# Performance work log

Hardware: AMD Instinct MI355X
Metric: run time of the kernel (lower is better)

The kernel has to match this reference:

```python
import jax, jax.numpy as jnp
import numpy as np

NUM_SPLITS = 2  # attn_splits


def _split_c_last(x, ns):
    # split_feature(channel_last=True): [b,h,w,c] -> [b*ns*ns, h/ns, w/ns, c]
    b, h, w, c = x.shape
    x = x.reshape(b, ns, h // ns, ns, w // ns, c)
    x = jnp.transpose(x, (0, 1, 3, 2, 4, 5))
    return x.reshape(b * ns * ns, h // ns, w // ns, c)


def _merge_c_last(x, ns):
    # merge_splits(channel_last=True): [b*ns*ns, hh, ww, c] -> [b, ns*hh, ns*ww, c]
    bn, hh, ww, c = x.shape
    b = bn // (ns * ns)
    x = x.reshape(b, ns, ns, hh, ww, c)
    x = jnp.transpose(x, (0, 1, 3, 2, 4, 5))
    return x.reshape(b, ns * hh, ns * ww, c)


def _make_shift_window_mask(h, w, ns):
    # exact port of generate_shift_window_attn_mask (numpy, setup-time only)
    wh, ww = h // ns, w // ns
    sh, sw = wh // 2, ww // 2
    img = np.zeros((h, w))
    cnt = 0
    for hs in (slice(0, -wh), slice(-wh, -sh), slice(-sh, None)):
        for ws in (slice(0, -ww), slice(-ww, -sw), slice(-sw, None)):
            img[hs, ws] = cnt
            cnt += 1
    mw = img.reshape(ns, wh, ns, ww).transpose(0, 2, 1, 3).reshape(ns * ns, wh * ww)
    am = mw[:, None, :] - mw[:, :, None]  # [n, i, j] = mw[n, j] - mw[n, i]
    am = np.where(am != 0, -100.0, 0.0).astype(np.float32)
    return jnp.asarray(am)


def _window_attention(q, k, v, attn_mask, h, w, ns):
    # single_head_split_window_attention with with_shift=True
    b, hw, c = q.shape
    sh, sw = (h // ns) // 2, (w // ns) // 2

    def prep(x):
        x = x.reshape(b, h, w, c)
        x = jnp.roll(x, shift=(-sh, -sw), axis=(1, 2))
        return _split_c_last(x, ns).reshape(b * ns * ns, -1, c)

    qs, ks, vs = prep(q), prep(k), prep(v)
    scale = jnp.asarray(c, q.dtype) ** 0.5
    scores = jnp.einsum('bqc,bkc->bqk', qs, ks) / scale
    scores = scores + jnp.tile(attn_mask, (b, 1, 1))
    attn = jax.nn.softmax(scores, axis=-1)
    out = jnp.einsum('bqk,bkc->bqc', attn, vs)
    out = _merge_c_last(out.reshape(b * ns * ns, h // ns, w // ns, c), ns)
    out = jnp.roll(out, shift=(sh, sw), axis=(1, 2))
    return out.reshape(b, hw, c)


def _global_correlation_softmax(feature0, feature1):
    b, c, h, w = feature0.shape
    hw = h * w
    f0 = feature0.reshape(b, c, hw).transpose(0, 2, 1)  # [b, hw, c]
    f1 = feature1.reshape(b, c, hw)                     # [b, c, hw]
    scale = jnp.asarray(c, feature0.dtype) ** 0.5
    corr = jnp.matmul(f0, f1) / scale                   # [b, hw, hw]

    yy, xx = jnp.meshgrid(jnp.arange(h), jnp.arange(w), indexing='ij')
    init_grid = jnp.stack([xx, yy], axis=0).astype(feature0.dtype)  # [2,h,w]
    init_grid = jnp.broadcast_to(init_grid[None], (b, 2, h, w))
    grid = init_grid.reshape(b, 2, hw).transpose(0, 2, 1)            # [b, hw, 2]

    corr2 = jnp.concatenate([corr, jnp.transpose(corr, (0, 2, 1))], axis=0)  # [2b,hw,hw]
    grid2 = jnp.tile(grid, (2, 1, 1))
    init2 = jnp.tile(init_grid, (2, 1, 1, 1))

    prob = jax.nn.softmax(corr2, axis=-1)
    corresp = jnp.matmul(prob, grid2).reshape(2 * b, h, w, 2)
    corresp = jnp.transpose(corresp, (0, 3, 1, 2))
    flow = corresp - init2
    f01, f10 = flow[:b], flow[b:]
    dual_prob = prob[:b] * jnp.transpose(prob[b:], (0, 2, 1))
    return f01, f10, dual_prob


def setup_inputs() -> dict:
    key = jax.random.key(0)
    b, c, h, w = 2, 128, 48, 96
    ks = jax.random.split(key, 5)
    q = jax.random.normal(ks[0], (b, h * w, c), dtype=jnp.float32)
    k = jax.random.normal(ks[1], (b, h * w, c), dtype=jnp.float32)
    v = jax.random.normal(ks[2], (b, h * w, c), dtype=jnp.float32)
    feature0 = jax.random.normal(ks[3], (b, c, h, w), dtype=jnp.float32)
    feature1 = jax.random.normal(ks[4], (b, c, h, w), dtype=jnp.float32)
    attn_mask = _make_shift_window_mask(h, w, NUM_SPLITS)
    return {"q": q, "k": k, "v": v, "feature0": feature0, "feature1": feature1,
            "attn_mask": attn_mask, "h": h, "w": w}


def reference(q, k, v, feature0, feature1, attn_mask, h, w):
    attn_out = _window_attention(q, k, v, attn_mask, h, w, NUM_SPLITS)
    f01, f10, dual_prob = _global_correlation_softmax(feature0, feature1)
    return (attn_out, f01, f10, dual_prob)
```

## Files before the change

kernel.cpp:

```cpp
#include <hip/hip_runtime.h>

#define HW 4608
#define CC 128
#define H 48
#define W 96
#define S_WIN 1152
#define SCALE 0.08838834764831845f

typedef __attribute__((ext_vector_type(8))) short bf16x8;
typedef __attribute__((ext_vector_type(4))) float f32x4;

static __device__ inline short f2bf(float f) {
    unsigned u = __builtin_bit_cast(unsigned, f);
    unsigned r = (u + 0x7fff + ((u >> 16) & 1)) >> 16;
    return (short)r;
}

__global__ __launch_bounds__(256)
void prep_all(const float* __restrict__ Q, const float* __restrict__ K, const float* __restrict__ V,
              const float* __restrict__ f0, const float* __restrict__ f1,
              bf16x8* __restrict__ cfragA, bf16x8* __restrict__ cfragB,
              bf16x8* __restrict__ qfrag, bf16x8* __restrict__ kfrag, bf16x8* __restrict__ vfrag,
              float* __restrict__ wsf)
{
    __shared__ float vt[32][132];
    const int bx = blockIdx.x;
    const int t = threadIdx.x;

    if (bx < 1152) {
        int zi = bx * 256 + t;
        if (zi < 12 * HW) wsf[zi] = 0.f;
        const int pt = bx % 72;
        const int z  = bx / 72;
        const int tensor = z >> 3, b = (z >> 2) & 1, kc = z & 3;
        const float* src = (tensor ? f1 : f0) + (size_t)b * CC * HW + (size_t)kc * 32 * HW + pt * 64;
        {
            int ch = t >> 4;
            int c4 = (t & 15) * 4;
            *(float4*)&vt[ch][c4]      = *(const float4*)&src[(size_t)ch * HW + c4];
            *(float4*)&vt[ch + 16][c4] = *(const float4*)&src[(size_t)(ch + 16) * HW + c4];
        }
        __syncthreads();
        int Rloc = t >> 6, lane = t & 63;
        int R = pt * 4 + Rloc;
        bf16x8 v;
        #pragma unroll
        for (int j = 0; j < 8; ++j) v[j] = f2bf(vt[(lane >> 4) * 8 + j][Rloc * 16 + (lane & 15)]);
        (tensor ? cfragB : cfragA)[((size_t)(b * 288 + R) * 4 + kc) * 64 + lane] = v;
    } else {
        const int bx2 = bx - 1152;
        const int R2 = bx2 % 36;
        const int z  = bx2 / 36;
        const int tensor = z >> 3, wb = z & 7;
        const int bb = wb >> 2, wi = wb & 3, si = wi >> 1, sj = wi & 1;
        const float* src = (tensor == 0 ? Q : (tensor == 1 ? K : V)) + (size_t)bb * HW * CC;
        {
            int row = t >> 3;
            int c16 = (t & 7) * 16;
            int qw = R2 * 32 + row;
            int rr = qw / 48, cc = qw - rr * 48;
            int y = (si * 24 + rr + 12) % 48;
            int x = (sj * 48 + cc + 24) % 96;
            const float* rp = src + ((size_t)y * 96 + x) * CC + c16;
            #pragma unroll
            for (int u = 0; u < 4; ++u)
                *(float4*)&vt[row][c16 + u * 4] = *(const float4*)&rp[u * 4];
        }
        __syncthreads();
        if (tensor < 2) {
            bf16x8* frag = tensor == 0 ? qfrag : kfrag;
            #pragma unroll
            for (int e2 = 0; e2 < 2; ++e2) {
                int e = t + e2 * 256;
                int Rloc = e >> 8, kc = (e >> 6) & 3, lane = e & 63;
                int R = R2 * 2 + Rloc;
                bf16x8 v;
                #pragma unroll
                for (int j = 0; j < 8; ++j)
                    v[j] = f2bf(vt[Rloc * 16 + (lane & 15)][kc * 32 + (lane >> 4) * 8 + j]);
                frag[((size_t)(wb * 72 + R) * 4 + kc) * 64 + lane] = v;
            }
        } else {
            #pragma unroll
            for (int e2 = 0; e2 < 2; ++e2) {
                int e = t + e2 * 256;
                int dB = e >> 6, lane = e & 63;
                bf16x8 v;
                #pragma unroll
                for (int j = 0; j < 8; ++j)
                    v[j] = f2bf(vt[(lane >> 4) * 8 + j][dB * 16 + (lane & 15)]);
                vfrag[((size_t)(wb * 8 + dB) * 36 + R2) * 64 + lane] = v;
            }
        }
    }
}

__global__ __launch_bounds__(512)
void win_attn(const bf16x8* __restrict__ qfrag, const bf16x8* __restrict__ kfrag,
              const bf16x8* __restrict__ vfrag, float* __restrict__ out)
{
    __shared__ __align__(16) short Psh[16 * 1152];
    __shared__ unsigned char codes[S_WIN];
    __shared__ float rsum_sh[16];

    const int t = threadIdx.x, lane = t & 63, w = t >> 6;
    const int qt = blockIdx.x;
    const int wb = blockIdx.y;
    const int bb = wb >> 2, wi = wb & 3, si = wi >> 1, sj = wi & 1;

    if (t < 16) rsum_sh[t] = 0.f;
    for (int i = t; i < S_WIN; i += 512) {
        int r = i / 48, c = i - r * 48;
        codes[i] = (unsigned char)((si ? (r >= 12) : 0) | ((sj ? (c >= 24) : 0) << 1));
    }
    __syncthreads();

    bf16x8 qf[4];
    {
        const bf16x8* qb = qfrag + ((size_t)(wb * 72 + qt) * 4) * 64 + lane;
        #pragma unroll
        for (int kc = 0; kc < 4; ++kc) qf[kc] = qb[kc * 64];
    }
    const int qcode = codes[qt * 16 + (lane & 15)];
    char* Pb = (char*)Psh;
    float rsum = 0.f;

    for (int kt = 0; kt < 9; ++kt) {
        int Rk = w * 9 + kt;
        const bf16x8* kb = kfrag + ((size_t)(wb * 72 + Rk) * 4) * 64 + lane;
        bf16x8 kf[4];
        #pragma unroll
        for (int kc = 0; kc < 4; ++kc) kf[kc] = kb[kc * 64];
        int k0 = Rk * 16 + (lane >> 4) * 4;
        f32x4 acc = {0.f, 0.f, 0.f, 0.f};
        #pragma unroll
        for (int kc = 0; kc < 4; ++kc)
            acc = __builtin_amdgcn_mfma_f32_16x16x32_bf16(kf[kc], qf[kc], acc, 0, 0, 0);
        float ev[4];
        #pragma unroll
        for (int r = 0; r < 4; ++r) {
            ev[r] = (codes[k0 + r] == qcode) ? __expf(acc[r] * SCALE) : 0.f;
            rsum += ev[r];
        }
        unsigned lo = (unsigned)(unsigned short)f2bf(ev[0]) | ((unsigned)(unsigned short)f2bf(ev[1]) << 16);
        unsigned hi = (unsigned)(unsigned short)f2bf(ev[2]) | ((unsigned)(unsigned short)f2bf(ev[3]) << 16);
        int qloc = lane & 15;
        int off = (qloc * 2304 + k0 * 2) ^ ((qloc & 7) << 4);
        *(uint2*)(Pb + off) = make_uint2(lo, hi);
    }
    rsum += __shfl_xor(rsum, 16); rsum += __shfl_xor(rsum, 32);
    if (lane < 16) atomicAdd(&rsum_sh[lane], rsum);
    __syncthreads();

    f32x4 pv = {0.f, 0.f, 0.f, 0.f};
    const bf16x8* vb = vfrag + ((size_t)(wb * 8 + w) * 36) * 64 + lane;
    for (int kc = 0; kc < 36; ++kc) {
        int qloc = lane & 15;
        int off = (qloc * 2304 + kc * 64 + (lane >> 4) * 16) ^ ((qloc & 7) << 4);
        bf16x8 pf = *(const bf16x8*)(Pb + off);
        pv = __builtin_amdgcn_mfma_f32_16x16x32_bf16(pf, vb[kc * 64], pv, 0, 0, 0);
    }
    #pragma unroll
    for (int r = 0; r < 4; ++r) {
        int qloc = (lane >> 4) * 4 + r;
        float val = pv[r] / rsum_sh[qloc];
        int qw = qt * 16 + qloc;
        int rr = qw / 48, cc2 = qw - rr * 48;
        int y = (si * 24 + rr + 12) % 48;
        int x = (sj * 48 + cc2 + 24) % 96;
        out[((size_t)bb * HW + y * 96 + x) * CC + w * 16 + (lane & 15)] = val;
    }
}

__global__ __launch_bounds__(256)
void corr_stats(const bf16x8* __restrict__ fragA, const bf16x8* __restrict__ fragB,
                float* __restrict__ rowsum, float* __restrict__ colsum)
{
    __shared__ float rs[128], cs[128];
    const int t = threadIdx.x, lane = t & 63, wave = t >> 6;
    const int wm = wave >> 1, wn = wave & 1;
    const int kt = blockIdx.x, qt = blockIdx.y, b = blockIdx.z;

    const bf16x8* Ab = fragA + (size_t)(b * 288 + qt * 8 + wm * 4) * 256 + lane;
    const bf16x8* Bb = fragB + (size_t)(b * 288 + kt * 8 + wn * 4) * 256 + lane;

    f32x4 acc[4][4] = {};
    #pragma unroll
    for (int kc = 0; kc < 4; ++kc) {
        bf16x8 a[4], bf[4];
        #pragma unroll
        for (int m = 0; m < 4; ++m) a[m]  = Ab[(m * 4 + kc) * 64];
        #pragma unroll
        for (int n = 0; n < 4; ++n) bf[n] = Bb[(n * 4 + kc) * 64];
        #pragma unroll
        for (int m = 0; m < 4; ++m)
            #pragma unroll
            for (int n = 0; n < 4; ++n)
                acc[m][n] = __builtin_amdgcn_mfma_f32_16x16x32_bf16(a[m], bf[n], acc[m][n], 0, 0, 0);
    }

    if (t < 128) { rs[t] = 0.f; cs[t] = 0.f; }
    __syncthreads();

    float cv[4] = {};
    #pragma unroll
    for (int m = 0; m < 4; ++m) {
        float rv[4] = {};
        #pragma unroll
        for (int n = 0; n < 4; ++n)
            #pragma unroll
            for (int r = 0; r < 4; ++r) {
                float ev = __expf(acc[m][n][r] * SCALE);
                rv[r] += ev; cv[n] += ev;
            }
        #pragma unroll
        for (int r = 0; r < 4; ++r) {
            float s = rv[r];
            s += __shfl_xor(s, 1); s += __shfl_xor(s, 2);
            s += __shfl_xor(s, 4); s += __shfl_xor(s, 8);
            if ((lane & 15) == 0)
                atomicAdd(&rs[wm * 64 + m * 16 + (lane >> 4) * 4 + r], s);
        }
    }
    #pragma unroll
    for (int n = 0; n < 4; ++n) {
        float s = cv[n];
        s += __shfl_xor(s, 16); s += __shfl_xor(s, 32);
        if (lane < 16) atomicAdd(&cs[wn * 64 + n * 16 + lane], s);
    }
    __syncthreads();
    if (t < 128)      atomicAdd(&rowsum[(size_t)b * HW + qt * 128 + t], rs[t]);
    else              atomicAdd(&colsum[(size_t)b * HW + kt * 128 + (t - 128)], cs[t - 128]);
}

__global__ __launch_bounds__(256)
void corr_final(const bf16x8* __restrict__ fragA, const bf16x8* __restrict__ fragB,
                const float* __restrict__ rowsum, const float* __restrict__ colsum,
                float* __restrict__ rowflow, float* __restrict__ colflow,
                float* __restrict__ dual)
{
    __shared__ float sfx[128], sfy[128], scx[128], scy[128];
    __shared__ float stg[4][16][68];
    const int t = threadIdx.x, lane = t & 63, wave = t >> 6;
    const int wm = wave >> 1, wn = wave & 1;
    const int kt = blockIdx.x, qt = blockIdx.y, b = blockIdx.z;

    const bf16x8* Ab = fragA + (size_t)(b * 288 + qt * 8 + wm * 4) * 256 + lane;
    const bf16x8* Bb = fragB + (size_t)(b * 288 + kt * 8 + wn * 4) * 256 + lane;

    f32x4 acc[4][4] = {};
    #pragma unroll
    for (int kc = 0; kc < 4; ++kc) {
        bf16x8 a[4], bf[4];
        #pragma unroll
        for (int m = 0; m < 4; ++m) a[m]  = Ab[(m * 4 + kc) * 64];
        #pragma unroll
        for (int n = 0; n < 4; ++n) bf[n] = Bb[(n * 4 + kc) * 64];
        #pragma unroll
        for (int m = 0; m < 4; ++m)
            #pragma unroll
            for (int n = 0; n < 4; ++n)
                acc[m][n] = __builtin_amdgcn_mfma_f32_16x16x32_bf16(a[m], bf[n], acc[m][n], 0, 0, 0);
    }

    if (t < 128) { sfx[t] = 0.f; sfy[t] = 0.f; scx[t] = 0.f; scy[t] = 0.f; }
    __syncthreads();

    const int qbase = qt * 128 + wm * 64;
    const int kbase = kt * 128 + wn * 64;

    float cinv[4], gkx[4], gky[4];
    #pragma unroll
    for (int n = 0; n < 4; ++n) {
        int k = kbase + n * 16 + (lane & 15);
        cinv[n] = 1.f / colsum[(size_t)b * HW + k];
        int kyi = k / W;
        gkx[n] = (float)(k - kyi * W); gky[n] = (float)kyi;
    }

    float cfx[4] = {}, cfy[4] = {};
    #pragma unroll
    for (int m = 0; m < 4; ++m) {
        float rinv[4], gqx[4], gqy[4];
        int q0 = qbase + m * 16 + (lane >> 4) * 4;
        #pragma unroll
        for (int r = 0; r < 4; ++r) {
            rinv[r] = 1.f / rowsum[(size_t)b * HW + q0 + r];
            int qyi = (q0 + r) / W;
            gqx[r] = (float)(q0 + r - qyi * W); gqy[r] = (float)qyi;
        }
        float rfx[4] = {}, rfy[4] = {};
        #pragma unroll
        for (int n = 0; n < 4; ++n) {
            #pragma unroll
            for (int r = 0; r < 4; ++r) {
                float ev = __expf(acc[m][n][r] * SCALE);
                float rp = ev * rinv[r];
                float ce = ev * cinv[n];
                stg[wave][(lane >> 4) * 4 + r][n * 16 + (lane & 15)] = rp * ce;
                rfx[r] += rp * gkx[n]; rfy[r] += rp * gky[n];
                cfx[n] += ce * gqx[r]; cfy[n] += ce * gqy[r];
            }
        }
        #pragma unroll
        for (int pass = 0; pass < 4; ++pass) {
            int row = pass * 4 + (lane >> 4);
            float4 vv = *(const float4*)&stg[wave][row][(lane & 15) * 4];
            *(float4*)&dual[((size_t)b * HW + qbase + m * 16 + row) * HW + kbase + (lane & 15) * 4] = vv;
        }
        #pragma unroll
        for (int r = 0; r < 4; ++r) {
            float sx = rfx[r], sy = rfy[r];
            sx += __shfl_xor(sx, 1); sx += __shfl_xor(sx, 2);
            sx += __shfl_xor(sx, 4); sx += __shfl_xor(sx, 8);
            sy += __shfl_xor(sy, 1); sy += __shfl_xor(sy, 2);
            sy += __shfl_xor(sy, 4); sy += __shfl_xor(sy, 8);
            if ((lane & 15) == 0) {
                int row = wm * 64 + m * 16 + (lane >> 4) * 4 + r;
                atomicAdd(&sfx[row], sx); atomicAdd(&sfy[row], sy);
            }
        }
    }
    #pragma unroll
    for (int n = 0; n < 4; ++n) {
        float sx = cfx[n], sy = cfy[n];
        sx += __shfl_xor(sx, 16); sx += __shfl_xor(sx, 32);
        sy += __shfl_xor(sy, 16); sy += __shfl_xor(sy, 32);
        if (lane < 16) {
            int col = wn * 64 + n * 16 + lane;
            atomicAdd(&scx[col], sx); atomicAdd(&scy[col], sy);
        }
    }
    __syncthreads();
    if (t < 128) {
        atomicAdd(&rowflow[((size_t)b * HW + qt * 128 + t) * 2 + 0], sfx[t]);
        atomicAdd(&rowflow[((size_t)b * HW + qt * 128 + t) * 2 + 1], sfy[t]);
    } else {
        int j = t - 128;
        atomicAdd(&colflow[((size_t)b * HW + kt * 128 + j) * 2 + 0], scx[j]);
        atomicAdd(&colflow[((size_t)b * HW + kt * 128 + j) * 2 + 1], scy[j]);
    }
}

__global__ void flow_finalize(const float* __restrict__ rowflow, const float* __restrict__ colflow,
                              float* __restrict__ out)
{
    int i = blockIdx.x * 256 + threadIdx.x;
    if (i >= 2 * 2 * HW) return;
    int bb   = i / (2 * HW);
    int rem  = i % (2 * HW);
    int chan = rem / HW;
    int q    = rem % HW;
    float g = (chan == 0) ? (float)(q % W) : (float)(q / W);
    out[i]              = rowflow[((size_t)bb * HW + q) * 2 + chan] - g;
    out[2 * 2 * HW + i] = colflow[((size_t)bb * HW + q) * 2 + chan] - g;
}

extern "C" void kernel_launch(void* const* d_in, const int* in_sizes, int n_in,
                              void* d_out, int out_size, void* d_ws, size_t ws_size,
                              hipStream_t stream)
{
    (void)in_sizes; (void)n_in; (void)out_size; (void)ws_size;
    const float* q  = (const float*)d_in[0];
    const float* k  = (const float*)d_in[1];
    const float* v  = (const float*)d_in[2];
    const float* f0 = (const float*)d_in[3];
    const float* f1 = (const float*)d_in[4];

    float* out = (float*)d_out;
    const size_t ATTN_SZ = (size_t)2 * HW * CC;
    const size_t FLOW_SZ = (size_t)2 * 2 * HW;
    float* f01  = out + ATTN_SZ;
    float* dual = out + ATTN_SZ + 2 * FLOW_SZ;

    const size_t FR = 2359296;
    char* wsb = (char*)d_ws;
    bf16x8* cfragA = (bf16x8*)(wsb);
    bf16x8* cfragB = (bf16x8*)(wsb + FR);
    bf16x8* qfrag  = (bf16x8*)(wsb + 2 * FR);
    bf16x8* kfrag  = (bf16x8*)(wsb + 3 * FR);
    bf16x8* vfrag  = (bf16x8*)(wsb + 4 * FR);
    float* wsf     = (float*)(wsb + 5 * FR);
    float* rowsum  = wsf;
    float* colsum  = wsf + 2 * HW;
    float* rowflow = wsf + 4 * HW;
    float* colflow = wsf + 8 * HW;

    prep_all<<<dim3(2016), 256, 0, stream>>>(q, k, v, f0, f1, cfragA, cfragB,
                                             qfrag, kfrag, vfrag, wsf);
    win_attn<<<dim3(72, 8), 512, 0, stream>>>(qfrag, kfrag, vfrag, out);
    corr_stats<<<dim3(36, 36, 2), 256, 0, stream>>>(cfragA, cfragB, rowsum, colsum);
    corr_final<<<dim3(36, 36, 2), 256, 0, stream>>>(cfragA, cfragB, rowsum, colsum,
                                                    rowflow, colflow, dual);
    flow_finalize<<<dim3(72), 256, 0, stream>>>(rowflow, colflow, f01);
}
```

Baseline: 133.8 us.

## Merge window attention and correlation stats into one launch; nontemporal dual stores

Combines the window-attention kernel and the correlation row/column-sum kernel into a single launch by splitting the block index range. The attention part now runs 256 threads per block, with each wave doing twice the key tiles and two output column tiles. This removes one launch and lets the two independent workloads fill the GPU together. Separately, the large dual-probability output is written with nontemporal stores to reduce cache pollution. The fused kernel's register pressure and shared-memory footprint apply to both halves, which may change occupancy.

```diff
diff --git a/kernel.cpp b/kernel.cpp
--- a/kernel.cpp
+++ b/kernel.cpp
@@ -95,142 +95,147 @@
     }
 }
 
-__global__ __launch_bounds__(512)
-void win_attn(const bf16x8* __restrict__ qfrag, const bf16x8* __restrict__ kfrag,
-              const bf16x8* __restrict__ vfrag, float* __restrict__ out)
+__global__ __launch_bounds__(256)
+void fused_ws(const bf16x8* __restrict__ qfrag, const bf16x8* __restrict__ kfrag,
+              const bf16x8* __restrict__ vfrag, float* __restrict__ out,
+              const bf16x8* __restrict__ cfragA, const bf16x8* __restrict__ cfragB,
+              float* __restrict__ rowsum, float* __restrict__ colsum)
 {
-    __shared__ __align__(16) short Psh[16 * 1152];
-    __shared__ unsigned char codes[S_WIN];
-    __shared__ float rsum_sh[16];
-
+    __shared__ __align__(16) char smem[38144];
+    const int bx = blockIdx.x;
     const int t = threadIdx.x, lane = t & 63, w = t >> 6;
-    const int qt = blockIdx.x;
-    const int wb = blockIdx.y;
-    const int bb = wb >> 2, wi = wb & 3, si = wi >> 1, sj = wi & 1;
-
-    if (t < 16) rsum_sh[t] = 0.f;
-    for (int i = t; i < S_WIN; i += 512) {
-        int r = i / 48, c = i - r * 48;
-        codes[i] = (unsigned char)((si ? (r >= 12) : 0) | ((sj ? (c >= 24) : 0) << 1));
-    }
-    __syncthreads();
-
-    bf16x8 qf[4];
-    {
-        const bf16x8* qb = qfrag + ((size_t)(wb * 72 + qt) * 4) * 64 + lane;
-        #pragma unroll
-        for (int kc = 0; kc < 4; ++kc) qf[kc] = qb[kc * 64];
-    }
-    const int qcode = codes[qt * 16 + (lane & 15)];
-    char* Pb = (char*)Psh;
-    float rsum = 0.f;
-
-    for (int kt = 0; kt < 9; ++kt) {
-        int Rk = w * 9 + kt;
-        const bf16x8* kb = kfrag + ((size_t)(wb * 72 + Rk) * 4) * 64 + lane;
-        bf16x8 kf[4];
-        #pragma unroll
-        for (int kc = 0; kc < 4; ++kc) kf[kc] = kb[kc * 64];
-        int k0 = Rk * 16 + (lane >> 4) * 4;
-        f32x4 acc = {0.f, 0.f, 0.f, 0.f};
-        #pragma unroll
-        for (int kc = 0; kc < 4; ++kc)
-            acc = __builtin_amdgcn_mfma_f32_16x16x32_bf16(kf[kc], qf[kc], acc, 0, 0, 0);
-        float ev[4];
+
+    if (bx < 576) {
+        short* Psh = (short*)smem;
+        unsigned char* codes = (unsigned char*)(smem + 36864);
+        float* rsum_sh = (float*)(smem + 38016);
+        const int qt = bx % 72, wb = bx / 72;
+        const int bb = wb >> 2, wi = wb & 3, si = wi >> 1, sj = wi & 1;
+
+        if (t < 16) rsum_sh[t] = 0.f;
+        for (int i = t; i < S_WIN; i += 256) {
+            int r = i / 48, c = i - r * 48;
+            codes[i] = (unsigned char)((si ? (r >= 12) : 0) | ((sj ? (c >= 24) : 0) << 1));
+        }
+        __syncthreads();
+
+        bf16x8 qf[4];
+        {
+            const bf16x8* qb = qfrag + ((size_t)(wb * 72 + qt) * 4) * 64 + lane;
+            #pragma unroll
+            for (int kc = 0; kc < 4; ++kc) qf[kc] = qb[kc * 64];
+        }
+        const int qcode = codes[qt * 16 + (lane & 15)];
+        char* Pb = (char*)Psh;
+        float rsum = 0.f;
+
+        for (int kt = 0; kt < 18; ++kt) {
+            int Rk = w * 18 + kt;
+            const bf16x8* kb = kfrag + ((size_t)(wb * 72 + Rk) * 4) * 64 + lane;
+            bf16x8 kf[4];
+            #pragma unroll
+            for (int kc = 0; kc < 4; ++kc) kf[kc] = kb[kc * 64];
+            int k0 = Rk * 16 + (lane >> 4) * 4;
+            f32x4 acc = {0.f, 0.f, 0.f, 0.f};
+            #pragma unroll
+            for (int kc = 0; kc < 4; ++kc)
+                acc = __builtin_amdgcn_mfma_f32_16x16x32_bf16(kf[kc], qf[kc], acc, 0, 0, 0);
+            float ev[4];
+            #pragma unroll
+            for (int r = 0; r < 4; ++r) {
+                ev[r] = (codes[k0 + r] == qcode) ? __expf(acc[r] * SCALE) : 0.f;
+                rsum += ev[r];
+            }
+            unsigned lo = (unsigned)(unsigned short)f2bf(ev[0]) | ((unsigned)(unsigned short)f2bf(ev[1]) << 16);
+            unsigned hi = (unsigned)(unsigned short)f2bf(ev[2]) | ((unsigned)(unsigned short)f2bf(ev[3]) << 16);
+            int qloc = lane & 15;
+            int off = (qloc * 2304 + k0 * 2) ^ ((qloc & 7) << 4);
+            *(uint2*)(Pb + off) = make_uint2(lo, hi);
+        }
+        rsum += __shfl_xor(rsum, 16); rsum += __shfl_xor(rsum, 32);
+        if (lane < 16) atomicAdd(&rsum_sh[lane], rsum);
+        __syncthreads();
+
+        f32x4 pv0 = {0.f, 0.f, 0.f, 0.f}, pv1 = {0.f, 0.f, 0.f, 0.f};
+        const bf16x8* vb0 = vfrag + ((size_t)(wb * 8 + w) * 36) * 64 + lane;
+        const bf16x8* vb1 = vfrag + ((size_t)(wb * 8 + w + 4) * 36) * 64 + lane;
+        for (int kc = 0; kc < 36; ++kc) {
+            int qloc = lane & 15;
+            int off = (qloc * 2304 + kc * 64 + (lane >> 4) * 16) ^ ((qloc & 7) << 4);
+            bf16x8 pf = *(const bf16x8*)(Pb + off);
+            pv0 = __builtin_amdgcn_mfma_f32_16x16x32_bf16(pf, vb0[kc * 64], pv0, 0, 0, 0);
+            pv1 = __builtin_amdgcn_mfma_f32_16x16x32_bf16(pf, vb1[kc * 64], pv1, 0, 0, 0);
+        }
         #pragma unroll
         for (int r = 0; r < 4; ++r) {
-            ev[r] = (codes[k0 + r] == qcode) ? __expf(acc[r] * SCALE) : 0.f;
-            rsum += ev[r];
-        }
-        unsigned lo = (unsigned)(unsigned short)f2bf(ev[0]) | ((unsigned)(unsigned short)f2bf(ev[1]) << 16);
-        unsigned hi = (unsigned)(unsigned short)f2bf(ev[2]) | ((unsigned)(unsigned short)f2bf(ev[3]) << 16);
-        int qloc = lane & 15;
-        int off = (qloc * 2304 + k0 * 2) ^ ((qloc & 7) << 4);
-        *(uint2*)(Pb + off) = make_uint2(lo, hi);
-    }
-    rsum += __shfl_xor(rsum, 16); rsum += __shfl_xor(rsum, 32);
-    if (lane < 16) atomicAdd(&rsum_sh[lane], rsum);
-    __syncthreads();
-
-    f32x4 pv = {0.f, 0.f, 0.f, 0.f};
-    const bf16x8* vb = vfrag + ((size_t)(wb * 8 + w) * 36) * 64 + lane;
-    for (int kc = 0; kc < 36; ++kc) {
-        int qloc = lane & 15;
-        int off = (qloc * 2304 + kc * 64 + (lane >> 4) * 16) ^ ((qloc & 7) << 4);
-        bf16x8 pf = *(const bf16x8*)(Pb + off);
-        pv = __builtin_amdgcn_mfma_f32_16x16x32_bf16(pf, vb[kc * 64], pv, 0, 0, 0);
-    }
-    #pragma unroll
-    for (int r = 0; r < 4; ++r) {
-        int qloc = (lane >> 4) * 4 + r;
-        float val = pv[r] / rsum_sh[qloc];
-        int qw = qt * 16 + qloc;
-        int rr = qw / 48, cc2 = qw - rr * 48;
-        int y = (si * 24 + rr + 12) % 48;
-        int x = (sj * 48 + cc2 + 24) % 96;
-        out[((size_t)bb * HW + y * 96 + x) * CC + w * 16 + (lane & 15)] = val;
-    }
-}
-
-__global__ __launch_bounds__(256)
-void corr_stats(const bf16x8* __restrict__ fragA, const bf16x8* __restrict__ fragB,
-                float* __restrict__ rowsum, float* __restrict__ colsum)
-{
-    __shared__ float rs[128], cs[128];
-    const int t = threadIdx.x, lane = t & 63, wave = t >> 6;
-    const int wm = wave >> 1, wn = wave & 1;
-    const int kt = blockIdx.x, qt = blockIdx.y, b = blockIdx.z;
-
-    const bf16x8* Ab = fragA + (size_t)(b * 288 + qt * 8 + wm * 4) * 256 + lane;
-    const bf16x8* Bb = fragB + (size_t)(b * 288 + kt * 8 + wn * 4) * 256 + lane;
-
-    f32x4 acc[4][4] = {};
-    #pragma unroll
-    for (int kc = 0; kc < 4; ++kc) {
-        bf16x8 a[4], bf[4];
-        #pragma unroll
-        for (int m = 0; m < 4; ++m) a[m]  = Ab[(m * 4 + kc) * 64];
-        #pragma unroll
-        for (int n = 0; n < 4; ++n) bf[n] = Bb[(n * 4 + kc) * 64];
-        #pragma unroll
-        for (int m = 0; m < 4; ++m)
+            int qloc = (lane >> 4) * 4 + r;
+            float rinv = 1.f / rsum_sh[qloc];
+            int qw = qt * 16 + qloc;
+            int rr = qw / 48, cc2 = qw - rr * 48;
+            int y = (si * 24 + rr + 12) % 48;
+            int x = (sj * 48 + cc2 + 24) % 96;
+            float* op = &out[((size_t)bb * HW + y * 96 + x) * CC + (lane & 15)];
+            op[w * 16]       = pv0[r] * rinv;
+            op[(w + 4) * 16] = pv1[r] * rinv;
+        }
+    } else {
+        float* rs = (float*)smem;
+        float* cs = (float*)(smem + 512);
+        const int bx2 = bx - 576;
+        const int kt = bx2 % 36, qt = (bx2 / 36) % 36, b = bx2 / 1296;
+        const int wm = w >> 1, wn = w & 1;
+
+        const bf16x8* Ab = cfragA + (size_t)(b * 288 + qt * 8 + wm * 4) * 256 + lane;
+        const bf16x8* Bb = cfragB + (size_t)(b * 288 + kt * 8 + wn * 4) * 256 + lane;
+
+        f32x4 acc[4][4] = {};
+        #pragma unroll
+        for (int kc = 0; kc < 4; ++kc) {
+            bf16x8 a[4], bf[4];
+            #pragma unroll
+            for (int m = 0; m < 4; ++m) a[m]  = Ab[(m * 4 + kc) * 64];
+            #pragma unroll
+            for (int n = 0; n < 4; ++n) bf[n] = Bb[(n * 4 + kc) * 64];
+            #pragma unroll
+            for (int m = 0; m < 4; ++m)
+                #pragma unroll
+                for (int n = 0; n < 4; ++n)
+                    acc[m][n] = __builtin_amdgcn_mfma_f32_16x16x32_bf16(a[m], bf[n], acc[m][n], 0, 0, 0);
+        }
+
+        if (t < 128) { rs[t] = 0.f; cs[t] = 0.f; }
+        __syncthreads();
+
+        float cv[4] = {};
+        #pragma unroll
+        for (int m = 0; m < 4; ++m) {
+            float rv[4] = {};
             #pragma unroll
             for (int n = 0; n < 4; ++n)
-                acc[m][n] = __builtin_amdgcn_mfma_f32_16x16x32_bf16(a[m], bf[n], acc[m][n], 0, 0, 0);
-    }
-
-    if (t < 128) { rs[t] = 0.f; cs[t] = 0.f; }
-    __syncthreads();
-
-    float cv[4] = {};
-    #pragma unroll
-    for (int m = 0; m < 4; ++m) {
-        float rv[4] = {};
-        #pragma unroll
-        for (int n = 0; n < 4; ++n)
+                #pragma unroll
+                for (int r = 0; r < 4; ++r) {
+                    float ev = __expf(acc[m][n][r] * SCALE);
+                    rv[r] += ev; cv[n] += ev;
+                }
             #pragma unroll
             for (int r = 0; r < 4; ++r) {
-                float ev = __expf(acc[m][n][r] * SCALE);
-                rv[r] += ev; cv[n] += ev;
-            }
-        #pragma unroll
-        for (int r = 0; r < 4; ++r) {
-            float s = rv[r];
-            s += __shfl_xor(s, 1); s += __shfl_xor(s, 2);
-            s += __shfl_xor(s, 4); s += __shfl_xor(s, 8);
-            if ((lane & 15) == 0)
-                atomicAdd(&rs[wm * 64 + m * 16 + (lane >> 4) * 4 + r], s);
-        }
-    }
-    #pragma unroll
-    for (int n = 0; n < 4; ++n) {
-        float s = cv[n];
-        s += __shfl_xor(s, 16); s += __shfl_xor(s, 32);
-        if (lane < 16) atomicAdd(&cs[wn * 64 + n * 16 + lane], s);
-    }
-    __syncthreads();
-    if (t < 128)      atomicAdd(&rowsum[(size_t)b * HW + qt * 128 + t], rs[t]);
-    else              atomicAdd(&colsum[(size_t)b * HW + kt * 128 + (t - 128)], cs[t - 128]);
+                float s = rv[r];
+                s += __shfl_xor(s, 1); s += __shfl_xor(s, 2);
+                s += __shfl_xor(s, 4); s += __shfl_xor(s, 8);
+                if ((lane & 15) == 0)
+                    atomicAdd(&rs[wm * 64 + m * 16 + (lane >> 4) * 4 + r], s);
+            }
+        }
+        #pragma unroll
+        for (int n = 0; n < 4; ++n) {
+            float s = cv[n];
+            s += __shfl_xor(s, 16); s += __shfl_xor(s, 32);
+            if (lane < 16) atomicAdd(&cs[wn * 64 + n * 16 + lane], s);
+        }
+        __syncthreads();
+        if (t < 128)      atomicAdd(&rowsum[(size_t)b * HW + qt * 128 + t], rs[t]);
+        else              atomicAdd(&colsum[(size_t)b * HW + kt * 128 + (t - 128)], cs[t - 128]);
+    }
 }
 
 __global__ __launch_bounds__(256)
@@ -305,8 +310,9 @@
         #pragma unroll
         for (int pass = 0; pass < 4; ++pass) {
             int row = pass * 4 + (lane >> 4);
-            float4 vv = *(const float4*)&stg[wave][row][(lane & 15) * 4];
-            *(float4*)&dual[((size_t)b * HW + qbase + m * 16 + row) * HW + kbase + (lane & 15) * 4] = vv;
+            f32x4 vv = *(const f32x4*)&stg[wave][row][(lane & 15) * 4];
+            __builtin_nontemporal_store(vv,
+                (f32x4*)&dual[((size_t)b * HW + qbase + m * 16 + row) * HW + kbase + (lane & 15) * 4]);
         }
         #pragma unroll
         for (int r = 0; r < 4; ++r) {
@@ -388,8 +394,8 @@
 
     prep_all<<<dim3(2016), 256, 0, stream>>>(q, k, v, f0, f1, cfragA, cfragB,
                                              qfrag, kfrag, vfrag, wsf);
-    win_attn<<<dim3(72, 8), 512, 0, stream>>>(qfrag, kfrag, vfrag, out);
-    corr_stats<<<dim3(36, 36, 2), 256, 0, stream>>>(cfragA, cfragB, rowsum, colsum);
+    fused_ws<<<dim3(576 + 2592), 256, 0, stream>>>(qfrag, kfrag, vfrag, out,
+                                                   cfragA, cfragB, rowsum, colsum);
     corr_final<<<dim3(36, 36, 2), 256, 0, stream>>>(cfragA, cfragB, rowsum, colsum,
                                                     rowflow, colflow, dual);
     flow_finalize<<<dim3(72), 256, 0, stream>>>(rowflow, colflow, f01);
```

Measured after the change: 113.7 us, median of 2. 15.0% less time.
